# Performance work log

Measured on AMD Instinct MI355X. Metric: run time of the kernel, lower is better.

The kernel has to match this reference:

```python
import jax, jax.numpy as jnp
import numpy as np

B = 262144          # batch of independent thermostat states
L = 64              # hidden width l
SIG_RANGE = 10.0    # SigmoidLinear range
T_ON = 66.0
T_OFF = 78.0
N_STEPS = 40        # While(target_idx=[0], test=40.0), step starts at 0


def setup_inputs() -> dict:
    key = jax.random.key(0)
    k0, k1, k2, k3, k4 = jax.random.split(key, 5)
    step = jnp.zeros((B,), jnp.float32)
    isOn = jnp.round(jax.random.uniform(k0, (B,), jnp.float32))
    temp = jax.random.uniform(k1, (B,), jnp.float32, minval=55.0, maxval=85.0)
    aux = jax.random.uniform(k2, (B,), jnp.float32)
    x_init = jnp.stack([step, isOn, temp, aux], axis=-1)  # [B, 4]
    W1 = jax.random.normal(k3, (2, L), jnp.float32) * 0.5
    b1 = jnp.zeros((L,), jnp.float32)
    W2 = jax.random.normal(k4, (L, 1), jnp.float32) * 0.5
    b2 = jnp.zeros((1,), jnp.float32)
    return {"x_init": x_init, "W1": W1, "b1": b1, "W2": W2, "b2": b2}


def _plant_nn(temp, aux, W1, b1, W2, b2):
    # LinearReLU: Linear(2->L) -> ReLU -> Linear(L->1) -> SigmoidLinear(sig_range)
    inp = jnp.stack([temp, aux], axis=-1)            # [B, 2]
    h = jax.nn.relu(inp @ W1 + b1)                   # [B, L]
    s = jax.nn.sigmoid(h @ W2 + b2)[..., 0]          # [B]
    return s * SIG_RANGE - SIG_RANGE / 2.0           # map to [-range/2, range/2]


def reference(x_init, W1, b1, W2, b2):
    def body(state, _):
        step = state[:, 0]
        isOn = state[:, 1]
        temp = state[:, 2]
        aux = state[:, 3]
        active = step < N_STEPS  # data-dependent while guard (masked scan)
        plant = _plant_nn(temp, aux, W1, b1, W2, b2)
        dtemp = plant * 10.0
        off = isOn <= 0.5
        # cooling branch (isOn <= 0.5): temp += plant*10; if temp <= tOn: isOn = 1
        # heating branch: temp += plant*10 + 5;        if temp >  tOff: isOn = 0
        temp_new = jnp.where(off, temp + dtemp, temp + dtemp + 5.0)
        isOn_new = jnp.where(
            off,
            jnp.where(temp_new <= T_ON, 1.0, isOn),
            jnp.where(temp_new <= T_OFF, isOn, 0.0),
        )
        temp2 = jnp.where(active, temp_new, temp)
        isOn2 = jnp.where(active, isOn_new, isOn)
        step2 = jnp.where(active, step + 1.0, step)
        new_state = jnp.stack([step2, isOn2, temp2, aux], axis=-1)
        return new_state, temp2  # Trajectory(target_idx=[2]) records temperature

    final_state, traj = jax.lax.scan(body, x_init, None, length=N_STEPS)
    return traj  # [N_STEPS, B] temperature trajectory
```

## Files before the change

kernel.cpp:

```cpp
#include <hip/hip_runtime.h>
#include <math.h>


#define LHID 64
#define NSTEPS 40

__global__ __launch_bounds__(256, 1) void thermostat_kernel(
    const float* __restrict__ x_init,
    const float* __restrict__ W1,
    const float* __restrict__ b1,
    const float* __restrict__ W2,
    const float* __restrict__ b2,
    float* __restrict__ out,
    int B)
{
    int b = blockIdx.x * blockDim.x + threadIdx.x;
    if (b >= B) return;

    float4 st = reinterpret_cast<const float4*>(x_init)[b];
    float step0 = st.x;
    float isOn  = st.y;
    float temp  = st.z;
    float aux   = st.w;
    float bias2 = b2[0];

    int n_active = (int)fminf(fmaxf((float)NSTEPS - step0, 0.0f), (float)NSTEPS);

    float a[LHID];
    float w2[LHID];
    float c[LHID];
#pragma unroll
    for (int j = 0; j < LHID; j += 4) {
        float4 va  = *reinterpret_cast<const float4*>(&W1[j]);
        float4 vr1 = *reinterpret_cast<const float4*>(&W1[LHID + j]);
        float4 vb  = *reinterpret_cast<const float4*>(&b1[j]);
        float4 vw2 = *reinterpret_cast<const float4*>(&W2[j]);
        a[j+0] = va.x;  a[j+1] = va.y;  a[j+2] = va.z;  a[j+3] = va.w;
        w2[j+0] = vw2.x; w2[j+1] = vw2.y; w2[j+2] = vw2.z; w2[j+3] = vw2.w;
        c[j+0] = fmaf(aux, vr1.x, vb.x);
        c[j+1] = fmaf(aux, vr1.y, vb.y);
        c[j+2] = fmaf(aux, vr1.z, vb.z);
        c[j+3] = fmaf(aux, vr1.w, vb.w);
    }
#pragma unroll
    for (int j = 0; j < LHID; ++j) {
        asm volatile("" : "+v"(a[j]));
        asm volatile("" : "+v"(w2[j]));
        asm volatile("" : "+v"(c[j]));
    }

#pragma unroll 1
    for (int t = 0; t < NSTEPS; ++t) {
        float acc = 0.0f;
#pragma unroll
        for (int j = 0; j < LHID; ++j) {
            float h = fmaf(temp, a[j], c[j]);
            h = fmaxf(h, 0.0f);
            acc = fmaf(h, w2[j], acc);
        }
        float x = __fadd_rn(acc, bias2);

        float e = expf(-fabsf(x));
        float s;
        if (x >= 0.0f) s = 1.0f / (1.0f + e);
        else           s = e / (1.0f + e);

        float plant = __fsub_rn(__fmul_rn(s, 10.0f), 5.0f);
        float dtemp = __fmul_rn(plant, 10.0f);

        float tn_off = __fadd_rn(temp, dtemp);
        float tn_on  = __fadd_rn(tn_off, 5.0f);

        bool off = (isOn <= 0.5f);
        float temp_new = off ? tn_off : tn_on;
        float isOn_new;
        if (off) isOn_new = (temp_new <= 66.0f) ? 1.0f : isOn;
        else     isOn_new = (temp_new <= 78.0f) ? isOn : 0.0f;

        if (t < n_active) {
            temp = temp_new;
            isOn = isOn_new;
        }

        out[(size_t)t * B + b] = temp;
    }
}

extern "C" void kernel_launch(void* const* d_in, const int* in_sizes, int n_in,
                              void* d_out, int out_size, void* d_ws, size_t ws_size,
                              hipStream_t stream) {
    const float* x_init = (const float*)d_in[0];
    const float* W1     = (const float*)d_in[1];
    const float* b1     = (const float*)d_in[2];
    const float* W2     = (const float*)d_in[3];
    const float* b2     = (const float*)d_in[4];
    float* out = (float*)d_out;

    int B = in_sizes[0] / 4;
    int threads = 256;
    int blocks = (B + threads - 1) / threads;
    thermostat_kernel<<<blocks, threads, 0, stream>>>(x_init, W1, b1, W2, b2, out, B);
}
```

Before: 58.82 us.

## Move shared W1/W2 weights into LDS to cut VGPRs and raise occupancy

Keeps the per-thread c[] array in registers but reads the uniform W1 row and W2 weights from LDS with float4 loads instead of holding them in VGPRs. Launch bounds now ask for 2 blocks per SM so more waves can hide latency. The sigmoid branch becomes a select, and the output pointer is advanced incrementally. The cost is LDS broadcast reads inside the hot inner loop in place of register operands.

```diff
diff --git a/kernel.cpp b/kernel.cpp
--- a/kernel.cpp
+++ b/kernel.cpp
@@ -5,7 +5,7 @@
 #define LHID 64
 #define NSTEPS 40
 
-__global__ __launch_bounds__(256, 1) void thermostat_kernel(
+__global__ __launch_bounds__(256, 2) void thermostat_kernel(
     const float* __restrict__ x_init,
     const float* __restrict__ W1,
     const float* __restrict__ b1,
@@ -14,7 +14,17 @@
     float* __restrict__ out,
     int B)
 {
-    int b = blockIdx.x * blockDim.x + threadIdx.x;
+    __shared__ __align__(16) float lds_a[LHID];
+    __shared__ __align__(16) float lds_w2[LHID];
+
+    int tid = threadIdx.x;
+    if (tid < LHID) {
+        lds_a[tid]  = W1[tid];
+        lds_w2[tid] = W2[tid];
+    }
+    __syncthreads();
+
+    int b = blockIdx.x * blockDim.x + tid;
     if (b >= B) return;
 
     float4 st = reinterpret_cast<const float4*>(x_init)[b];
@@ -24,19 +34,13 @@
     float aux   = st.w;
     float bias2 = b2[0];
 
-    int n_active = (int)fminf(fmaxf((float)NSTEPS - step0, 0.0f), (float)NSTEPS);
+    int n_active = (int)ceilf(fminf(fmaxf((float)NSTEPS - step0, 0.0f), (float)NSTEPS));
 
-    float a[LHID];
-    float w2[LHID];
     float c[LHID];
 #pragma unroll
     for (int j = 0; j < LHID; j += 4) {
-        float4 va  = *reinterpret_cast<const float4*>(&W1[j]);
         float4 vr1 = *reinterpret_cast<const float4*>(&W1[LHID + j]);
         float4 vb  = *reinterpret_cast<const float4*>(&b1[j]);
-        float4 vw2 = *reinterpret_cast<const float4*>(&W2[j]);
-        a[j+0] = va.x;  a[j+1] = va.y;  a[j+2] = va.z;  a[j+3] = va.w;
-        w2[j+0] = vw2.x; w2[j+1] = vw2.y; w2[j+2] = vw2.z; w2[j+3] = vw2.w;
         c[j+0] = fmaf(aux, vr1.x, vb.x);
         c[j+1] = fmaf(aux, vr1.y, vb.y);
         c[j+2] = fmaf(aux, vr1.z, vb.z);
@@ -44,26 +48,28 @@
     }
 #pragma unroll
     for (int j = 0; j < LHID; ++j) {
-        asm volatile("" : "+v"(a[j]));
-        asm volatile("" : "+v"(w2[j]));
         asm volatile("" : "+v"(c[j]));
     }
+
+    float* po = out + b;
 
 #pragma unroll 1
     for (int t = 0; t < NSTEPS; ++t) {
         float acc = 0.0f;
 #pragma unroll
-        for (int j = 0; j < LHID; ++j) {
-            float h = fmaf(temp, a[j], c[j]);
-            h = fmaxf(h, 0.0f);
-            acc = fmaf(h, w2[j], acc);
+        for (int j = 0; j < LHID; j += 4) {
+            float4 av = *reinterpret_cast<const float4*>(&lds_a[j]);
+            float4 wv = *reinterpret_cast<const float4*>(&lds_w2[j]);
+            float h0 = fmaxf(fmaf(temp, av.x, c[j+0]), 0.0f); acc = fmaf(h0, wv.x, acc);
+            float h1 = fmaxf(fmaf(temp, av.y, c[j+1]), 0.0f); acc = fmaf(h1, wv.y, acc);
+            float h2 = fmaxf(fmaf(temp, av.z, c[j+2]), 0.0f); acc = fmaf(h2, wv.z, acc);
+            float h3 = fmaxf(fmaf(temp, av.w, c[j+3]), 0.0f); acc = fmaf(h3, wv.w, acc);
         }
         float x = __fadd_rn(acc, bias2);
 
         float e = expf(-fabsf(x));
-        float s;
-        if (x >= 0.0f) s = 1.0f / (1.0f + e);
-        else           s = e / (1.0f + e);
+        float num = (x >= 0.0f) ? 1.0f : e;
+        float s = num / (1.0f + e);
 
         float plant = __fsub_rn(__fmul_rn(s, 10.0f), 5.0f);
         float dtemp = __fmul_rn(plant, 10.0f);
@@ -82,7 +88,8 @@
             isOn = isOn_new;
         }
 
-        out[(size_t)t * B + b] = temp;
+        *po = temp;
+        po += B;
     }
 }
 
```

Measured after the change: 55.51 us. 1.06x faster.
